# Kernel tuning notes

Hardware: AMD Instinct MI355X
Metric: run time of the kernel (lower is better)

Reference implementation:

```python
import jax, jax.numpy as jnp
import numpy as np

N_NODES = 50000
N_EDGES = 800000
IN_DIM = 128
HEADS = 4
OUT_DIM = 16
HD = HEADS * OUT_DIM  # 64
EDGE_DIM = 1
NEG_SLOPE = 0.2


def setup_inputs() -> dict:
    key = jax.random.key(0)
    ks = jax.random.split(key, 12)
    x = jax.random.normal(ks[0], (N_NODES, IN_DIM), dtype=jnp.float32)
    edge_index = jax.random.randint(ks[1], (2, N_EDGES), 0, N_NODES, dtype=jnp.int64)
    edge_attr = jax.random.uniform(ks[2], (N_EDGES, EDGE_DIM), dtype=jnp.float32)
    s = 0.1
    Wl = jax.random.normal(ks[3], (IN_DIM, HD), dtype=jnp.float32) * s
    bl = jax.random.normal(ks[4], (HD,), dtype=jnp.float32) * s
    Wr = jax.random.normal(ks[5], (IN_DIM, HD), dtype=jnp.float32) * s
    br = jax.random.normal(ks[6], (HD,), dtype=jnp.float32) * s
    We = jax.random.normal(ks[7], (EDGE_DIM, HD), dtype=jnp.float32) * s
    att = jax.random.normal(ks[8], (HEADS, OUT_DIM), dtype=jnp.float32) * s
    bias_out = jax.random.normal(ks[9], (HD,), dtype=jnp.float32) * s
    Wres = jax.random.normal(ks[10], (IN_DIM, HD), dtype=jnp.float32) * s
    bres = jax.random.normal(ks[11], (HD,), dtype=jnp.float32) * s
    return {"x": x, "edge_index": edge_index, "edge_attr": edge_attr,
            "Wl": Wl, "bl": bl, "Wr": Wr, "br": br, "We": We,
            "att": att, "bias_out": bias_out, "Wres": Wres, "bres": bres}


def _gatv2_layer(x, edge_index, edge_attr, Wl, bl, Wr, br, We, att, bias_out, Wres, bres):
    src, dst = edge_index[0], edge_index[1]
    # projections: [N, H, D]
    x_l = (x @ Wl + bl).reshape(N_NODES, HEADS, OUT_DIM)
    x_r = (x @ Wr + br).reshape(N_NODES, HEADS, OUT_DIM)
    edge_emb = (edge_attr @ We).reshape(N_EDGES, HEADS, OUT_DIM)
    # per-edge attention score (GATv2): a^T LeakyReLU(x_l[src] + x_r[dst] + e)
    x_j = x_l[src]                                   # [E, H, D] gather (source message)
    feat = x_j + x_r[dst] + edge_emb                 # [E, H, D]
    score = jnp.einsum('ehd,hd->eh', jax.nn.leaky_relu(feat, NEG_SLOPE), att)  # [E, H]
    # segment softmax over destination neighborhoods
    m = jax.ops.segment_max(score, dst, num_segments=N_NODES)   # [N, H]
    ex = jnp.exp(score - m[dst])                                 # [E, H]
    denom = jax.ops.segment_sum(ex, dst, num_segments=N_NODES)  # [N, H]
    alpha = ex / (denom[dst] + 1e-16)                            # [E, H]
    # scatter-add aggregation of weighted source messages
    out = jax.ops.segment_sum(alpha[:, :, None] * x_j, dst, num_segments=N_NODES)  # [N, H, D]
    out = out.reshape(N_NODES, HD) + bias_out        # concat heads + conv bias
    # residual (in_dim != out_features -> linear projection), then ELU
    out = out + (x @ Wres + bres)
    out = jax.nn.elu(out)
    return out, edge_index, alpha


def reference(x, edge_index, edge_attr, Wl, bl, Wr, br, We, att, bias_out, Wres, bres):
    return _gatv2_layer(x, edge_index, edge_attr, Wl, bl, Wr, br, We, att, bias_out, Wres, bres)
```

## Files before the change

kernel.cpp:

```cpp
#include <hip/hip_runtime.h>
#include <math.h>

#define N_NODES 50000
#define N_EDGES 800000
#define IN_DIM  128
#define HEADS   4
#define OUT_DIM 16
#define HD      64
#define NEG_SLOPE 0.2f
#define CAP     128
#define LOG2E   1.44269504088896340736f

__device__ __forceinline__ float hw_exp2(float x) {
    return __builtin_amdgcn_exp2f(x);
}

__global__ __launch_bounds__(256)
void k1_proj(const float* __restrict__ x,
             const float* __restrict__ Wl, const float* __restrict__ bl,
             const float* __restrict__ Wr, const float* __restrict__ br,
             const float* __restrict__ Wres, const float* __restrict__ bres,
             int* __restrict__ count,
             float* __restrict__ xl, float* __restrict__ xr,
             float* __restrict__ xres) {
    __shared__ float xsT[IN_DIM][36];
    const int base = blockIdx.x * 32;

    const int gid = blockIdx.x * 256 + threadIdx.x;
    if (gid < N_NODES) count[gid] = 0;

    {
        const float4* x4 = (const float4*)x;
#pragma unroll
        for (int r = 0; r < 4; ++r) {
            const int E    = threadIdx.x * 4 + r;
            const int node = E >> 5;
            const int kq   = E & 31;
            float4 v = make_float4(0.f, 0.f, 0.f, 0.f);
            if (base + node < N_NODES) v = x4[(size_t)(base + node) * 32 + kq];
            xsT[4 * kq + 0][node] = v.x;
            xsT[4 * kq + 1][node] = v.y;
            xsT[4 * kq + 2][node] = v.z;
            xsT[4 * kq + 3][node] = v.w;
        }
    }
    __syncthreads();

    const int lane = threadIdx.x & 63;
    const int wv   = threadIdx.x >> 6;
    const int u    = lane & 15;
    const int g    = lane >> 4;
    const int n0   = wv * 8;

    float4 aL[8], aR[8], aS[8];
#pragma unroll
    for (int i = 0; i < 8; ++i) {
        aL[i] = make_float4(0.f, 0.f, 0.f, 0.f);
        aR[i] = make_float4(0.f, 0.f, 0.f, 0.f);
        aS[i] = make_float4(0.f, 0.f, 0.f, 0.f);
    }

    const float* pL = Wl   + g * HD + 4 * u;
    const float* pR = Wr   + g * HD + 4 * u;
    const float* pS = Wres + g * HD + 4 * u;

#pragma unroll 2
    for (int k0 = 0; k0 < IN_DIM; k0 += 4) {
        const int k = k0 + g;
        const float4 wl4 = *(const float4*)(pL + k0 * HD);
        const float4 wr4 = *(const float4*)(pR + k0 * HD);
        const float4 ws4 = *(const float4*)(pS + k0 * HD);
        const float4 xa  = *(const float4*)&xsT[k][n0];
        const float4 xb  = *(const float4*)&xsT[k][n0 + 4];
        const float xn[8] = {xa.x, xa.y, xa.z, xa.w, xb.x, xb.y, xb.z, xb.w};
#pragma unroll
        for (int i = 0; i < 8; ++i) {
            aL[i].x += xn[i] * wl4.x; aL[i].y += xn[i] * wl4.y;
            aL[i].z += xn[i] * wl4.z; aL[i].w += xn[i] * wl4.w;
            aR[i].x += xn[i] * wr4.x; aR[i].y += xn[i] * wr4.y;
            aR[i].z += xn[i] * wr4.z; aR[i].w += xn[i] * wr4.w;
            aS[i].x += xn[i] * ws4.x; aS[i].y += xn[i] * ws4.y;
            aS[i].z += xn[i] * ws4.z; aS[i].w += xn[i] * ws4.w;
        }
    }

#pragma unroll
    for (int off = 16; off <= 32; off <<= 1) {
#pragma unroll
        for (int i = 0; i < 8; ++i) {
            aL[i].x += __shfl_xor(aL[i].x, off); aL[i].y += __shfl_xor(aL[i].y, off);
            aL[i].z += __shfl_xor(aL[i].z, off); aL[i].w += __shfl_xor(aL[i].w, off);
            aR[i].x += __shfl_xor(aR[i].x, off); aR[i].y += __shfl_xor(aR[i].y, off);
            aR[i].z += __shfl_xor(aR[i].z, off); aR[i].w += __shfl_xor(aR[i].w, off);
            aS[i].x += __shfl_xor(aS[i].x, off); aS[i].y += __shfl_xor(aS[i].y, off);
            aS[i].z += __shfl_xor(aS[i].z, off); aS[i].w += __shfl_xor(aS[i].w, off);
        }
    }

    if (g == 0) {
        const float4 bl4 = *(const float4*)(bl   + 4 * u);
        const float4 br4 = *(const float4*)(br   + 4 * u);
        const float4 bs4 = *(const float4*)(bres + 4 * u);
#pragma unroll
        for (int i = 0; i < 8; ++i) {
            const int node = base + n0 + i;
            if (node < N_NODES) {
                float4 o;
                const size_t off0 = (size_t)node * HD + 4 * u;
                o.x = aL[i].x + bl4.x; o.y = aL[i].y + bl4.y;
                o.z = aL[i].z + bl4.z; o.w = aL[i].w + bl4.w;
                *(float4*)(xl + off0) = o;
                o.x = aR[i].x + br4.x; o.y = aR[i].y + br4.y;
                o.z = aR[i].z + br4.z; o.w = aR[i].w + br4.w;
                *(float4*)(xr + off0) = o;
                o.x = aS[i].x + bs4.x; o.y = aS[i].y + bs4.y;
                o.z = aS[i].z + bs4.z; o.w = aS[i].w + bs4.w;
                *(float4*)(xres + off0) = o;
            }
        }
    }
}

__global__ __launch_bounds__(256)
void k2_hist(const int* __restrict__ dst, int* __restrict__ count) {
    int e = blockIdx.x * blockDim.x + threadIdx.x;
    if (e < N_EDGES) atomicAdd(&count[dst[e]], 1);
}

#define SCAN_BLOCKS 196

__global__ __launch_bounds__(256)
void k3a_scan1(const int* __restrict__ count, int* __restrict__ incl,
               int* __restrict__ bsum) {
    __shared__ int s[256];
    const int t = threadIdx.x;
    const int i = blockIdx.x * 256 + t;
    int c = (i < N_NODES) ? count[i] : 0;
    s[t] = c;
    __syncthreads();
    for (int off = 1; off < 256; off <<= 1) {
        int v = (t >= off) ? s[t - off] : 0;
        __syncthreads();
        s[t] += v;
        __syncthreads();
    }
    if (i < N_NODES) incl[i] = s[t];
    if (t == 255) bsum[blockIdx.x] = s[255];
}

__global__ __launch_bounds__(256)
void k3b_scan2(int* __restrict__ bsum, int* __restrict__ boff) {
    __shared__ int s[256];
    const int t = threadIdx.x;
    int c = (t < SCAN_BLOCKS) ? bsum[t] : 0;
    s[t] = c;
    __syncthreads();
    for (int off = 1; off < 256; off <<= 1) {
        int v = (t >= off) ? s[t - off] : 0;
        __syncthreads();
        s[t] += v;
        __syncthreads();
    }
    if (t < SCAN_BLOCKS) boff[t] = s[t] - c;
}

__global__ __launch_bounds__(256)
void k3c_scan3(const int* __restrict__ count, int* __restrict__ incl ,
               const int* __restrict__ boff, int* __restrict__ cursor) {
    const int i = blockIdx.x * 256 + threadIdx.x;
    if (i >= N_NODES) return;
    const int v = incl[i] - count[i] + boff[blockIdx.x];
    incl[i] = v;
    cursor[i] = v;
}

__global__ __launch_bounds__(256)
void k4_scatter(const int* __restrict__ src, const int* __restrict__ dst,
                const float* __restrict__ ea,
                int* __restrict__ cursor, int4* __restrict__ recs,
                float* __restrict__ out_ei) {
    int e = blockIdx.x * blockDim.x + threadIdx.x;
    if (e >= N_EDGES) return;
    const int d = dst[e];
    const int s = src[e];
    const int pos = atomicAdd(&cursor[d], 1);
    recs[pos] = make_int4(e, s, __float_as_int(ea[e]), 0);
    out_ei[e] = (float)s;
    out_ei[N_EDGES + e] = (float)d;
}

__global__ __launch_bounds__(256)
void k5_node(const int4* __restrict__ recs,
             const int* __restrict__ rowptr, const int* __restrict__ count,
             const float* __restrict__ xl, const float* __restrict__ xr,
             const float* __restrict__ xres,
             const float* __restrict__ We, const float* __restrict__ att,
             const float* __restrict__ bias_out,
             float* __restrict__ out, float* __restrict__ out_alpha) {
    __shared__ float sc_lds[4][CAP][HEADS];

    const int wv   = threadIdx.x >> 6;
    const int lane = threadIdx.x & 63;
    const int u    = lane & 15;
    const int g    = lane >> 4;
    const int n    = blockIdx.x * 4 + wv;

    const int base = rowptr[n];
    const int deg  = count[n];

    const float4 xr4 = *(const float4*)(xr  + (size_t)n * HD + 4 * u);
    const float4 We4 = *(const float4*)(We  + 4 * u);
    float4 at4       = *(const float4*)(att + 4 * u);
    at4.x *= LOG2E; at4.y *= LOG2E; at4.z *= LOG2E; at4.w *= LOG2E;

    float m = -INFINITY, dsum = 0.f;
    float4 acc = make_float4(0.f, 0.f, 0.f, 0.f);

    for (int c0 = 0; c0 < deg; c0 += 64) {
        const int nrem = min(64, deg - c0);
        int s_my = 0; float a_my = 0.f;
        if (lane < nrem) {
            const int4 r = recs[base + c0 + lane];
            s_my = r.y;
            a_my = __int_as_float(r.z);
        }
        const int nchunk = (nrem + 3) >> 2;

        int   j   = g;
        bool  v   = j < nrem;
        int   s   = __shfl(s_my, j);
        float aev = __shfl(a_my, j);
        float4 xlv = make_float4(0.f, 0.f, 0.f, 0.f);
        if (v) xlv = *(const float4*)(xl + (size_t)s * HD + 4 * u);

        for (int c = 0; c < nchunk; ++c) {
            const float4 cur  = xlv;
            const bool   curv = v;
            const float  ca   = aev;
            const int    cj   = 4 * c + g;
            j = 4 * (c + 1) + g;
            v = j < nrem;
            s   = __shfl(s_my, j & 63);
            aev = __shfl(a_my, j & 63);
            if (v) xlv = *(const float4*)(xl + (size_t)s * HD + 4 * u);

            if (curv) {
                float f0 = cur.x + xr4.x + ca * We4.x;
                float f1 = cur.y + xr4.y + ca * We4.y;
                float f2 = cur.z + xr4.z + ca * We4.z;
                float f3 = cur.w + xr4.w + ca * We4.w;
                f0 = f0 > 0.f ? f0 : NEG_SLOPE * f0;
                f1 = f1 > 0.f ? f1 : NEG_SLOPE * f1;
                f2 = f2 > 0.f ? f2 : NEG_SLOPE * f2;
                f3 = f3 > 0.f ? f3 : NEG_SLOPE * f3;
                float p = f0 * at4.x + f1 * at4.y + f2 * at4.z + f3 * at4.w;
                p += __shfl_xor(p, 1);
                p += __shfl_xor(p, 2);
                const int jj = c0 + cj;
                if (jj < CAP && (u & 3) == 0) sc_lds[wv][jj][u >> 2] = p;
                const float t    = hw_exp2(-fabsf(p - m));
                const bool  up   = (p >= m);
                const float scl  = up ? t : 1.f;
                const float pe   = up ? 1.f : t;
                m = fmaxf(m, p);
                dsum  = dsum * scl + pe;
                acc.x = acc.x * scl + pe * cur.x;
                acc.y = acc.y * scl + pe * cur.y;
                acc.z = acc.z * scl + pe * cur.z;
                acc.w = acc.w * scl + pe * cur.w;
            }
        }
    }

#pragma unroll
    for (int off = 16; off <= 32; off <<= 1) {
        const float mo = __shfl_xor(m, off);
        const float d2 = __shfl_xor(dsum, off);
        float4 a2;
        a2.x = __shfl_xor(acc.x, off);
        a2.y = __shfl_xor(acc.y, off);
        a2.z = __shfl_xor(acc.z, off);
        a2.w = __shfl_xor(acc.w, off);
        const float mm = fmaxf(m, mo);
        const float s1 = (m  == -INFINITY) ? 0.f : hw_exp2(m - mm);
        const float s2 = (mo == -INFINITY) ? 0.f : hw_exp2(mo - mm);
        dsum  = dsum * s1 + d2 * s2;
        acc.x = acc.x * s1 + a2.x * s2;
        acc.y = acc.y * s1 + a2.y * s2;
        acc.z = acc.z * s1 + a2.z * s2;
        acc.w = acc.w * s1 + a2.w * s2;
        m = mm;
    }
    const float inv = 1.f / (dsum + 1e-16f);

    const float m0 = __shfl(m, 0),  m1 = __shfl(m, 4);
    const float m2 = __shfl(m, 8),  m3 = __shfl(m, 12);
    const float i0 = __shfl(inv, 0), i1 = __shfl(inv, 4);
    const float i2 = __shfl(inv, 8), i3 = __shfl(inv, 12);

    __syncthreads();

    for (int jj = lane; jj < deg; jj += 64) {
        const int4 r = recs[base + jj];
        const int  e = r.x;
        float s0, s1, s2, s3;
        if (jj < CAP) {
            const float4 sc4 = *(const float4*)&sc_lds[wv][jj][0];
            s0 = sc4.x; s1 = sc4.y; s2 = sc4.z; s3 = sc4.w;
        } else {
            const int   sN  = r.y;
            const float aev = __int_as_float(r.z);
            float sc[4];
            for (int h2 = 0; h2 < 4; ++h2) {
                float a2 = 0.f;
                for (int d2 = 0; d2 < 16; ++d2) {
                    const int hd2 = h2 * 16 + d2;
                    float f = xl[(size_t)sN * HD + hd2] + xr[(size_t)n * HD + hd2]
                              + aev * We[hd2];
                    f = f > 0.f ? f : NEG_SLOPE * f;
                    a2 += f * att[hd2];
                }
                sc[h2] = a2 * LOG2E;
            }
            s0 = sc[0]; s1 = sc[1]; s2 = sc[2]; s3 = sc[3];
        }
        float4 a4;
        a4.x = hw_exp2(s0 - m0) * i0;
        a4.y = hw_exp2(s1 - m1) * i1;
        a4.z = hw_exp2(s2 - m2) * i2;
        a4.w = hw_exp2(s3 - m3) * i3;
        *(float4*)(out_alpha + (size_t)e * HEADS) = a4;
    }

    if (g == 0) {
        const float4 xs4 = *(const float4*)(xres + (size_t)n * HD + 4 * u);
        const float4 b4  = *(const float4*)(bias_out + 4 * u);
        float4 o;
        o.x = acc.x * inv + b4.x + xs4.x;
        o.y = acc.y * inv + b4.y + xs4.y;
        o.z = acc.z * inv + b4.z + xs4.z;
        o.w = acc.w * inv + b4.w + xs4.w;
        o.x = o.x > 0.f ? o.x : __expf(o.x) - 1.f;
        o.y = o.y > 0.f ? o.y : __expf(o.y) - 1.f;
        o.z = o.z > 0.f ? o.z : __expf(o.z) - 1.f;
        o.w = o.w > 0.f ? o.w : __expf(o.w) - 1.f;
        *(float4*)(out + (size_t)n * HD + 4 * u) = o;
    }
}

extern "C" void kernel_launch(void* const* d_in, const int* in_sizes, int n_in,
                              void* d_out, int out_size, void* d_ws, size_t ws_size,
                              hipStream_t stream) {
    const float* x        = (const float*)d_in[0];
    const int*   ei       = (const int*)d_in[1];
    const float* ea       = (const float*)d_in[2];
    const float* Wl       = (const float*)d_in[3];
    const float* bl       = (const float*)d_in[4];
    const float* Wr       = (const float*)d_in[5];
    const float* br       = (const float*)d_in[6];
    const float* We       = (const float*)d_in[7];
    const float* att      = (const float*)d_in[8];
    const float* bias_out = (const float*)d_in[9];
    const float* Wres     = (const float*)d_in[10];
    const float* bres     = (const float*)d_in[11];

    const int* src = ei;
    const int* dst = ei + N_EDGES;

    float* out       = (float*)d_out;
    float* out_ei    = out + (size_t)N_NODES * HD;
    float* out_alpha = out_ei + 2 * (size_t)N_EDGES;

    float* ws   = (float*)d_ws;
    float* xl   = ws;
    float* xr   = xl + (size_t)N_NODES * HD;
    float* xres = xr + (size_t)N_NODES * HD;
    int* ibuf   = (int*)(xres + (size_t)N_NODES * HD);
    int* count  = ibuf;
    int* rowptr = count + N_NODES;
    int* cursor = rowptr + N_NODES;
    int* bsum   = cursor + N_NODES;
    int* boff   = bsum + SCAN_BLOCKS;
    size_t recoff = (size_t)(boff + SCAN_BLOCKS - (int*)d_ws);
    recoff = (recoff + 3) & ~(size_t)3;
    int4* recs  = (int4*)((int*)d_ws + recoff);

    k1_proj<<<(N_NODES + 31) / 32, 256, 0, stream>>>(x, Wl, bl, Wr, br, Wres, bres,
                                                     count, xl, xr, xres);
    k2_hist<<<N_EDGES / 256, 256, 0, stream>>>(dst, count);
    k3a_scan1<<<SCAN_BLOCKS, 256, 0, stream>>>(count, rowptr, bsum);
    k3b_scan2<<<1, 256, 0, stream>>>(bsum, boff);
    k3c_scan3<<<SCAN_BLOCKS, 256, 0, stream>>>(count, rowptr, boff, cursor);
    k4_scatter<<<(N_EDGES + 255) / 256, 256, 0, stream>>>(src, dst, ea, cursor,
                                                          recs, out_ei);
    k5_node<<<N_NODES / 4, 256, 0, stream>>>(recs, rowptr, count,
                                             xl, xr, xres, We, att, bias_out,
                                             out, out_alpha);
}
```

Before: 317.6 us.

## Record per-edge rank in histogram and process 8 edges per wave

The histogram kernel now saves the return value of its atomic increment as a per-edge rank, so the scatter kernel computes each CSR position as rowptr plus rank and no longer needs a second atomic pass or a cursor array. In the node kernel, each lane now handles 8 features instead of 4, so a wave works on 8 neighbour edges at a time rather than 4. That halves the trip count for low-degree nodes and removes one shuffle from the score reduction. The cost is an extra 800K-int rank buffer written and read, and more registers per lane in the node kernel.

```diff
diff --git a/kernel.cpp b/kernel.cpp
--- a/kernel.cpp
+++ b/kernel.cpp
@@ -122,9 +122,10 @@
 }
 
 __global__ __launch_bounds__(256)
-void k2_hist(const int* __restrict__ dst, int* __restrict__ count) {
+void k2_hist(const int* __restrict__ dst, int* __restrict__ count,
+             int* __restrict__ rank) {
     int e = blockIdx.x * blockDim.x + threadIdx.x;
-    if (e < N_EDGES) atomicAdd(&count[dst[e]], 1);
+    if (e < N_EDGES) rank[e] = atomicAdd(&count[dst[e]], 1);
 }
 
 #define SCAN_BLOCKS 196
@@ -166,24 +167,22 @@
 
 __global__ __launch_bounds__(256)
 void k3c_scan3(const int* __restrict__ count, int* __restrict__ incl ,
-               const int* __restrict__ boff, int* __restrict__ cursor) {
+               const int* __restrict__ boff) {
     const int i = blockIdx.x * 256 + threadIdx.x;
     if (i >= N_NODES) return;
-    const int v = incl[i] - count[i] + boff[blockIdx.x];
-    incl[i] = v;
-    cursor[i] = v;
+    incl[i] = incl[i] - count[i] + boff[blockIdx.x];
 }
 
 __global__ __launch_bounds__(256)
 void k4_scatter(const int* __restrict__ src, const int* __restrict__ dst,
-                const float* __restrict__ ea,
-                int* __restrict__ cursor, int4* __restrict__ recs,
+                const float* __restrict__ ea, const int* __restrict__ rank,
+                const int* __restrict__ rowptr, int4* __restrict__ recs,
                 float* __restrict__ out_ei) {
     int e = blockIdx.x * blockDim.x + threadIdx.x;
     if (e >= N_EDGES) return;
     const int d = dst[e];
     const int s = src[e];
-    const int pos = atomicAdd(&cursor[d], 1);
+    const int pos = rowptr[d] + rank[e];
     recs[pos] = make_int4(e, s, __float_as_int(ea[e]), 0);
     out_ei[e] = (float)s;
     out_ei[N_EDGES + e] = (float)d;
@@ -201,20 +200,25 @@
 
     const int wv   = threadIdx.x >> 6;
     const int lane = threadIdx.x & 63;
-    const int u    = lane & 15;
-    const int g    = lane >> 4;
+    const int u    = lane & 7;
+    const int g    = lane >> 3;
     const int n    = blockIdx.x * 4 + wv;
 
     const int base = rowptr[n];
     const int deg  = count[n];
 
-    const float4 xr4 = *(const float4*)(xr  + (size_t)n * HD + 4 * u);
-    const float4 We4 = *(const float4*)(We  + 4 * u);
-    float4 at4       = *(const float4*)(att + 4 * u);
-    at4.x *= LOG2E; at4.y *= LOG2E; at4.z *= LOG2E; at4.w *= LOG2E;
+    const float4 xrA = *(const float4*)(xr + (size_t)n * HD + 8 * u);
+    const float4 xrB = *(const float4*)(xr + (size_t)n * HD + 8 * u + 4);
+    const float4 WeA = *(const float4*)(We + 8 * u);
+    const float4 WeB = *(const float4*)(We + 8 * u + 4);
+    float4 atA = *(const float4*)(att + 8 * u);
+    float4 atB = *(const float4*)(att + 8 * u + 4);
+    atA.x *= LOG2E; atA.y *= LOG2E; atA.z *= LOG2E; atA.w *= LOG2E;
+    atB.x *= LOG2E; atB.y *= LOG2E; atB.z *= LOG2E; atB.w *= LOG2E;
 
     float m = -INFINITY, dsum = 0.f;
-    float4 acc = make_float4(0.f, 0.f, 0.f, 0.f);
+    float4 accA = make_float4(0.f, 0.f, 0.f, 0.f);
+    float4 accB = make_float4(0.f, 0.f, 0.f, 0.f);
 
     for (int c0 = 0; c0 < deg; c0 += 64) {
         const int nrem = min(64, deg - c0);
@@ -224,79 +228,98 @@
             s_my = r.y;
             a_my = __int_as_float(r.z);
         }
-        const int nchunk = (nrem + 3) >> 2;
+        const int nchunk = (nrem + 7) >> 3;
 
         int   j   = g;
         bool  v   = j < nrem;
         int   s   = __shfl(s_my, j);
         float aev = __shfl(a_my, j);
-        float4 xlv = make_float4(0.f, 0.f, 0.f, 0.f);
-        if (v) xlv = *(const float4*)(xl + (size_t)s * HD + 4 * u);
+        float4 xlA = make_float4(0.f, 0.f, 0.f, 0.f);
+        float4 xlB = make_float4(0.f, 0.f, 0.f, 0.f);
+        if (v) {
+            xlA = *(const float4*)(xl + (size_t)s * HD + 8 * u);
+            xlB = *(const float4*)(xl + (size_t)s * HD + 8 * u + 4);
+        }
 
         for (int c = 0; c < nchunk; ++c) {
-            const float4 cur  = xlv;
+            const float4 curA = xlA, curB = xlB;
             const bool   curv = v;
             const float  ca   = aev;
-            const int    cj   = 4 * c + g;
-            j = 4 * (c + 1) + g;
+            const int    cj   = 8 * c + g;
+            j = 8 * (c + 1) + g;
             v = j < nrem;
             s   = __shfl(s_my, j & 63);
             aev = __shfl(a_my, j & 63);
-            if (v) xlv = *(const float4*)(xl + (size_t)s * HD + 4 * u);
+            if (v) {
+                xlA = *(const float4*)(xl + (size_t)s * HD + 8 * u);
+                xlB = *(const float4*)(xl + (size_t)s * HD + 8 * u + 4);
+            }
 
             if (curv) {
-                float f0 = cur.x + xr4.x + ca * We4.x;
-                float f1 = cur.y + xr4.y + ca * We4.y;
-                float f2 = cur.z + xr4.z + ca * We4.z;
-                float f3 = cur.w + xr4.w + ca * We4.w;
+                float f0 = curA.x + xrA.x + ca * WeA.x;
+                float f1 = curA.y + xrA.y + ca * WeA.y;
+                float f2 = curA.z + xrA.z + ca * WeA.z;
+                float f3 = curA.w + xrA.w + ca * WeA.w;
+                float f4 = curB.x + xrB.x + ca * WeB.x;
+                float f5 = curB.y + xrB.y + ca * WeB.y;
+                float f6 = curB.z + xrB.z + ca * WeB.z;
+                float f7 = curB.w + xrB.w + ca * WeB.w;
                 f0 = f0 > 0.f ? f0 : NEG_SLOPE * f0;
                 f1 = f1 > 0.f ? f1 : NEG_SLOPE * f1;
                 f2 = f2 > 0.f ? f2 : NEG_SLOPE * f2;
                 f3 = f3 > 0.f ? f3 : NEG_SLOPE * f3;
-                float p = f0 * at4.x + f1 * at4.y + f2 * at4.z + f3 * at4.w;
+                f4 = f4 > 0.f ? f4 : NEG_SLOPE * f4;
+                f5 = f5 > 0.f ? f5 : NEG_SLOPE * f5;
+                f6 = f6 > 0.f ? f6 : NEG_SLOPE * f6;
+                f7 = f7 > 0.f ? f7 : NEG_SLOPE * f7;
+                float p = f0 * atA.x + f1 * atA.y + f2 * atA.z + f3 * atA.w
+                        + f4 * atB.x + f5 * atB.y + f6 * atB.z + f7 * atB.w;
                 p += __shfl_xor(p, 1);
-                p += __shfl_xor(p, 2);
                 const int jj = c0 + cj;
-                if (jj < CAP && (u & 3) == 0) sc_lds[wv][jj][u >> 2] = p;
+                if (jj < CAP && (u & 1) == 0) sc_lds[wv][jj][u >> 1] = p;
                 const float t    = hw_exp2(-fabsf(p - m));
                 const bool  up   = (p >= m);
                 const float scl  = up ? t : 1.f;
                 const float pe   = up ? 1.f : t;
                 m = fmaxf(m, p);
                 dsum  = dsum * scl + pe;
-                acc.x = acc.x * scl + pe * cur.x;
-                acc.y = acc.y * scl + pe * cur.y;
-                acc.z = acc.z * scl + pe * cur.z;
-                acc.w = acc.w * scl + pe * cur.w;
+                accA.x = accA.x * scl + pe * curA.x;
+                accA.y = accA.y * scl + pe * curA.y;
+                accA.z = accA.z * scl + pe * curA.z;
+                accA.w = accA.w * scl + pe * curA.w;
+                accB.x = accB.x * scl + pe * curB.x;
+                accB.y = accB.y * scl + pe * curB.y;
+                accB.z = accB.z * scl + pe * curB.z;
+                accB.w = accB.w * scl + pe * curB.w;
             }
         }
     }
 
 #pragma unroll
-    for (int off = 16; off <= 32; off <<= 1) {
+    for (int off = 8; off <= 32; off <<= 1) {
         const float mo = __shfl_xor(m, off);
         const float d2 = __shfl_xor(dsum, off);
-        float4 a2;
-        a2.x = __shfl_xor(acc.x, off);
-        a2.y = __shfl_xor(acc.y, off);
-        a2.z = __shfl_xor(acc.z, off);
-        a2.w = __shfl_xor(acc.w, off);
+        float4 aA, aB;
+        aA.x = __shfl_xor(accA.x, off); aA.y = __shfl_xor(accA.y, off);
+        aA.z = __shfl_xor(accA.z, off); aA.w = __shfl_xor(accA.w, off);
+        aB.x = __shfl_xor(accB.x, off); aB.y = __shfl_xor(accB.y, off);
+        aB.z = __shfl_xor(accB.z, off); aB.w = __shfl_xor(accB.w, off);
         const float mm = fmaxf(m, mo);
         const float s1 = (m  == -INFINITY) ? 0.f : hw_exp2(m - mm);
         const float s2 = (mo == -INFINITY) ? 0.f : hw_exp2(mo - mm);
         dsum  = dsum * s1 + d2 * s2;
-        acc.x = acc.x * s1 + a2.x * s2;
-        acc.y = acc.y * s1 + a2.y * s2;
-        acc.z = acc.z * s1 + a2.z * s2;
-        acc.w = acc.w * s1 + a2.w * s2;
+        accA.x = accA.x * s1 + aA.x * s2; accA.y = accA.y * s1 + aA.y * s2;
+        accA.z = accA.z * s1 + aA.z * s2; accA.w = accA.w * s1 + aA.w * s2;
+        accB.x = accB.x * s1 + aB.x * s2; accB.y = accB.y * s1 + aB.y * s2;
+        accB.z = accB.z * s1 + aB.z * s2; accB.w = accB.w * s1 + aB.w * s2;
         m = mm;
     }
     const float inv = 1.f / (dsum + 1e-16f);
 
-    const float m0 = __shfl(m, 0),  m1 = __shfl(m, 4);
-    const float m2 = __shfl(m, 8),  m3 = __shfl(m, 12);
-    const float i0 = __shfl(inv, 0), i1 = __shfl(inv, 4);
-    const float i2 = __shfl(inv, 8), i3 = __shfl(inv, 12);
+    const float m0 = __shfl(m, 0),  m1 = __shfl(m, 2);
+    const float m2 = __shfl(m, 4),  m3 = __shfl(m, 6);
+    const float i0 = __shfl(inv, 0), i1 = __shfl(inv, 2);
+    const float i2 = __shfl(inv, 4), i3 = __shfl(inv, 6);
 
     __syncthreads();
 
@@ -333,18 +356,29 @@
     }
 
     if (g == 0) {
-        const float4 xs4 = *(const float4*)(xres + (size_t)n * HD + 4 * u);
-        const float4 b4  = *(const float4*)(bias_out + 4 * u);
+        const float4 xsA = *(const float4*)(xres + (size_t)n * HD + 8 * u);
+        const float4 xsB = *(const float4*)(xres + (size_t)n * HD + 8 * u + 4);
+        const float4 bA  = *(const float4*)(bias_out + 8 * u);
+        const float4 bB  = *(const float4*)(bias_out + 8 * u + 4);
         float4 o;
-        o.x = acc.x * inv + b4.x + xs4.x;
-        o.y = acc.y * inv + b4.y + xs4.y;
-        o.z = acc.z * inv + b4.z + xs4.z;
-        o.w = acc.w * inv + b4.w + xs4.w;
+        o.x = accA.x * inv + bA.x + xsA.x;
+        o.y = accA.y * inv + bA.y + xsA.y;
+        o.z = accA.z * inv + bA.z + xsA.z;
+        o.w = accA.w * inv + bA.w + xsA.w;
         o.x = o.x > 0.f ? o.x : __expf(o.x) - 1.f;
         o.y = o.y > 0.f ? o.y : __expf(o.y) - 1.f;
         o.z = o.z > 0.f ? o.z : __expf(o.z) - 1.f;
         o.w = o.w > 0.f ? o.w : __expf(o.w) - 1.f;
-        *(float4*)(out + (size_t)n * HD + 4 * u) = o;
+        *(float4*)(out + (size_t)n * HD + 8 * u) = o;
+        o.x = accB.x * inv + bB.x + xsB.x;
+        o.y = accB.y * inv + bB.y + xsB.y;
+        o.z = accB.z * inv + bB.z + xsB.z;
+        o.w = accB.w * inv + bB.w + xsB.w;
+        o.x = o.x > 0.f ? o.x : __expf(o.x) - 1.f;
+        o.y = o.y > 0.f ? o.y : __expf(o.y) - 1.f;
+        o.z = o.z > 0.f ? o.z : __expf(o.z) - 1.f;
+        o.w = o.w > 0.f ? o.w : __expf(o.w) - 1.f;
+        *(float4*)(out + (size_t)n * HD + 8 * u + 4) = o;
     }
 }
 
@@ -378,21 +412,21 @@
     int* ibuf   = (int*)(xres + (size_t)N_NODES * HD);
     int* count  = ibuf;
     int* rowptr = count + N_NODES;
-    int* cursor = rowptr + N_NODES;
-    int* bsum   = cursor + N_NODES;
+    int* bsum   = rowptr + N_NODES;
     int* boff   = bsum + SCAN_BLOCKS;
-    size_t recoff = (size_t)(boff + SCAN_BLOCKS - (int*)d_ws);
+    int* rank   = boff + SCAN_BLOCKS;
+    size_t recoff = (size_t)(rank + N_EDGES - (int*)d_ws);
     recoff = (recoff + 3) & ~(size_t)3;
     int4* recs  = (int4*)((int*)d_ws + recoff);
 
     k1_proj<<<(N_NODES + 31) / 32, 256, 0, stream>>>(x, Wl, bl, Wr, br, Wres, bres,
                                                      count, xl, xr, xres);
-    k2_hist<<<N_EDGES / 256, 256, 0, stream>>>(dst, count);
+    k2_hist<<<N_EDGES / 256, 256, 0, stream>>>(dst, count, rank);
     k3a_scan1<<<SCAN_BLOCKS, 256, 0, stream>>>(count, rowptr, bsum);
     k3b_scan2<<<1, 256, 0, stream>>>(bsum, boff);
-    k3c_scan3<<<SCAN_BLOCKS, 256, 0, stream>>>(count, rowptr, boff, cursor);
-    k4_scatter<<<(N_EDGES + 255) / 256, 256, 0, stream>>>(src, dst, ea, cursor,
-                                                          recs, out_ei);
+    k3c_scan3<<<SCAN_BLOCKS, 256, 0, stream>>>(count, rowptr, boff);
+    k4_scatter<<<(N_EDGES + 255) / 256, 256, 0, stream>>>(src, dst, ea, rank,
+                                                          rowptr, recs, out_ei);
     k5_node<<<N_NODES / 4, 256, 0, stream>>>(recs, rowptr, count,
                                              xl, xr, xres, We, att, bias_out,
                                              out, out_alpha);
```

New measurement: 268.6 us. -15.4%, faster.
